# Kernel optimization log

Measured on AMD Instinct MI355X. Metric: run time of the kernel, lower is better.

## Reference

```python
import jax, jax.numpy as jnp
import numpy as np
import math

D = 128  # embedding_dim, hard-coded in source


def setup_inputs() -> dict:
    key = jax.random.key(0)
    k1, k2, k3, k4, k5 = jax.random.split(key, 5)
    B, S = 4, 4096
    x = jax.random.normal(k1, (B, S, D), dtype=jnp.float32)
    token_attention_masks = jax.random.randint(k2, (B, S), 0, 2).astype(jnp.int64)
    # torch.rand -> uniform [0,1)
    w_query = jax.random.uniform(k3, (D, D), dtype=jnp.float32)
    w_key = jax.random.uniform(k4, (D, D), dtype=jnp.float32)
    w_value = jax.random.uniform(k5, (D, D), dtype=jnp.float32)
    return {
        "x": x,
        "token_attention_masks": token_attention_masks,
        "w_query": w_query,
        "w_key": w_key,
        "w_value": w_value,
    }


def reference(x, token_attention_masks, w_query, w_key, w_value):
    # QKV projections (single head, no bias)
    query = jnp.einsum('bsd,de->bse', x, w_query)
    key = jnp.einsum('bsd,de,->bse', x, w_key, jnp.float32(1.0)) if False else jnp.einsum('bsd,de->bse', x, w_key)
    value = jnp.einsum('bsd,de->bse', x, w_value)
    dk = key.shape[2]
    scale = jnp.einsum('bqd,bkd->bqk', query, key) / math.sqrt(dk)  # [B,S,S]
    # NOTE: the original module computes an additive mask (`new_scale`) but
    # applies softmax to the UNMASKED `scale` (a bug in the source); we
    # replicate the actual output math faithfully, so the mask is unused.
    attention_probability = jax.nn.softmax(scale, axis=2)
    attention_output = jnp.einsum('bqk,bkd->bqd', attention_probability, value)
    return attention_output
```

## Files before the change

kernel.cpp:

```cpp
#include <hip/hip_runtime.h>
#include <math.h>

#define BATCH  4
#define SEQ    4096
#define DIM    128
#define NROW   (BATCH*SEQ)
#define NSPLIT 8
#define NW     384

typedef _Float16 f16_t;
typedef _Float16 f16x4  __attribute__((ext_vector_type(4)));
typedef _Float16 f16x8  __attribute__((ext_vector_type(8)));
typedef _Float16 f16x16 __attribute__((ext_vector_type(16)));
typedef float    f32x4  __attribute__((ext_vector_type(4)));
typedef float    f32x16 __attribute__((ext_vector_type(16)));

#define QSCALE ((float)(1.4426950408889634 / 11.313708498984761))

__global__ __launch_bounds__(256) void wsplit_kernel(
    const float* __restrict__ wq, const float* __restrict__ wk,
    const float* __restrict__ wv,
    f16_t* __restrict__ Wth, f16_t* __restrict__ Wtl)
{
    const int idx = blockIdx.x*256 + threadIdx.x;
    const int n = idx >> 7;
    const int k = idx & 127;
    const int mat = n >> 7, col = n & 127;
    const float* w = (mat == 0) ? wq : ((mat == 1) ? wk : wv);
    const float v = w[k*DIM + col];
    const f16_t h = (f16_t)v;
    Wth[idx] = h;
    Wtl[idx] = (f16_t)(v - (float)h);
}

#define LDX 72
#define LDE 136

__global__ __launch_bounds__(256) void proj_kernel(
    const float* __restrict__ x,
    const f16_t* __restrict__ Wth, const f16_t* __restrict__ Wtl,
    f16_t* __restrict__ Qh, f16_t* __restrict__ Kh, f16_t* __restrict__ Vt)
{
    __shared__ __align__(16) f16_t smem[(64 + 64 + 128 + 128) * LDX];
    f16_t* sXh = smem;
    f16_t* sXl = smem + 64*LDX;
    f16_t* sWh = smem + 128*LDX;
    f16_t* sWl = smem + 256*LDX;

    const int tid  = threadIdx.x;
    const int wave = tid >> 6;
    const int lane = tid & 63;
    const int quad = lane >> 4;
    const int ln   = lane & 15;

    const int nt = blockIdx.x % 3;
    const int mb = blockIdx.x / 3;
    const int m0 = mb * 64;
    const int n0 = nt * 128;

    f32x4 acc[8];
    #pragma unroll
    for (int nb = 0; nb < 8; nb++)
        for (int r = 0; r < 4; r++) acc[nb][r] = 0.f;

    #pragma unroll
    for (int ph = 0; ph < 2; ph++) {
        __syncthreads();
        #pragma unroll
        for (int i = 0; i < 4; i++) {
            const int idx = tid + 256*i;
            const int r = idx >> 4, f4 = idx & 15;
            const float4 v = *(const float4*)(x + (size_t)(m0+r)*DIM + ph*64 + f4*4);
            f16_t h0=(f16_t)v.x, h1=(f16_t)v.y, h2=(f16_t)v.z, h3=(f16_t)v.w;
            *(f16x4*)(sXh + r*LDX + f4*4) = (f16x4){h0,h1,h2,h3};
            *(f16x4*)(sXl + r*LDX + f4*4) =
                (f16x4){(f16_t)(v.x-(float)h0),(f16_t)(v.y-(float)h1),
                        (f16_t)(v.z-(float)h2),(f16_t)(v.w-(float)h3)};
        }
        #pragma unroll
        for (int i = 0; i < 4; i++) {
            const int idx = tid + 256*i;
            const int n = idx >> 3, g = idx & 7;
            *(uint4*)(sWh + n*LDX + g*8) =
                *(const uint4*)(Wth + (size_t)(n0+n)*DIM + ph*64 + g*8);
            *(uint4*)(sWl + n*LDX + g*8) =
                *(const uint4*)(Wtl + (size_t)(n0+n)*DIM + ph*64 + g*8);
        }
        __syncthreads();

        f16x8 ah[2], al[2];
        #pragma unroll
        for (int ks = 0; ks < 2; ks++) {
            ah[ks] = *(const f16x8*)(sXh + (wave*16+ln)*LDX + quad*8 + ks*32);
            al[ks] = *(const f16x8*)(sXl + (wave*16+ln)*LDX + quad*8 + ks*32);
        }
        #pragma unroll
        for (int nb = 0; nb < 8; nb++) {
            #pragma unroll
            for (int ks = 0; ks < 2; ks++) {
                const f16x8 bh = *(const f16x8*)(sWh + (nb*16+ln)*LDX + quad*8 + ks*32);
                const f16x8 bl = *(const f16x8*)(sWl + (nb*16+ln)*LDX + quad*8 + ks*32);
                acc[nb] = __builtin_amdgcn_mfma_f32_16x16x32_f16(ah[ks], bh, acc[nb], 0,0,0);
                acc[nb] = __builtin_amdgcn_mfma_f32_16x16x32_f16(al[ks], bh, acc[nb], 0,0,0);
                acc[nb] = __builtin_amdgcn_mfma_f32_16x16x32_f16(ah[ks], bl, acc[nb], 0,0,0);
            }
        }
    }

    __syncthreads();

    if (nt != 2) {
        const float scale = (nt == 0) ? QSCALE : 1.0f;
        f16_t* dsth = (nt == 0) ? Qh : Kh;
        f16_t* sH = smem;
        #pragma unroll
        for (int nb = 0; nb < 8; nb++)
            #pragma unroll
            for (int r = 0; r < 4; r++) {
                const int row  = wave*16 + quad*4 + r;
                const int colp = (nb*16 + ln) ^ (quad << 4);
                sH[row*LDE + colp] = (f16_t)(acc[nb][r] * scale);
            }
        __syncthreads();
        #pragma unroll
        for (int jj = 0; jj < 4; jj++) {
            const int c    = tid + 256*jj;
            const int row  = c >> 4;
            const int col  = (c & 15) * 8;
            const int colp = col ^ (((row >> 2) & 3) << 4);
            *(uint4*)(dsth + (size_t)(m0 + row)*DIM + col) =
                *(const uint4*)(sH + row*LDE + colp);
        }
    } else {
        f16_t* svt = smem;
        const int rowl = wave*16 + quad*4;
        #pragma unroll
        for (int nb = 0; nb < 8; nb++)
            for (int r = 0; r < 4; r++)
                svt[(nb*16+ln)*LDX + rowl + r] = (f16_t)acc[nb][r];
        __syncthreads();
        const int bb = m0 >> 12, sloc = m0 & (SEQ-1);
        const int d = tid >> 1, half = tid & 1;
        #pragma unroll
        for (int q = 0; q < 4; q++) {
            *(uint4*)(Vt + ((size_t)bb*DIM + d)*SEQ + sloc + half*32 + q*8) =
                *(const uint4*)(svt + d*LDX + half*32 + q*8);
        }
    }
}

#define LDK 132
#define LDV 68
#define LDO 132

__global__ __launch_bounds__(256, 3) void flash_kernel(
    const f16_t* __restrict__ Qh, const f16_t* __restrict__ Kh,
    const f16_t* __restrict__ Vt,
    f16_t* __restrict__ Opart, float2* __restrict__ mlbuf)
{
    __shared__ __align__(16) f16_t smem[64*LDK + 128*LDV];
    f16_t* sK = smem;
    f16_t* sV = smem + 64*LDK;

    const int tid  = threadIdx.x;
    const int wave = tid >> 6;
    const int lane = tid & 63;
    const int l31  = lane & 31;
    const int h    = lane >> 5;

    const int grp = blockIdx.x & 31;
    const int b   = grp >> 3;
    const int sp  = grp & 7;
    const int qt  = blockIdx.x >> 5;
    const int q0  = qt*128 + wave*32;

    f16x8 qf[8];
    {
        const f16_t* gq = Qh + ((size_t)b*SEQ + q0 + l31)*DIM + h*8;
        #pragma unroll
        for (int ks = 0; ks < 8; ks++)
            qf[ks] = *(const f16x8*)(gq + ks*16);
    }

    f32x16 oacc[4];
    #pragma unroll
    for (int mb = 0; mb < 4; mb++)
        #pragma unroll
        for (int r = 0; r < 16; r++) oacc[mb][r] = 0.f;
    float mrun = -__builtin_inff(), lrun = 0.f;

    const int kr = tid >> 4;
    const int kc = (tid & 15) * 8;
    const int vd = tid >> 3;
    const int vj = (tid & 7) * 8;

    const f16_t* gK = Kh + (size_t)b*SEQ*DIM;
    const f16_t* gV = Vt + (size_t)b*DIM*SEQ;

    for (int kt = sp*8; kt < sp*8 + 8; kt++) {
        float4 pk[4], pv[4];
        {
            const f16_t* gk = gK + (size_t)kt*64*DIM;
            const f16_t* gv = gV + kt*64;
            #pragma unroll
            for (int p = 0; p < 4; p++)
                pk[p] = *(const float4*)(gk + (kr + 16*p)*DIM + kc);
            #pragma unroll
            for (int p = 0; p < 4; p++)
                pv[p] = *(const float4*)(gv + (size_t)(vd + 32*p)*SEQ + vj);
        }
        __syncthreads();
        #pragma unroll
        for (int p = 0; p < 4; p++) {
            const f16x8 w = __builtin_bit_cast(f16x8, pk[p]);
            *(f16x4*)(sK + (kr+16*p)*LDK + kc    ) = __builtin_shufflevector(w, w, 0,1,2,3);
            *(f16x4*)(sK + (kr+16*p)*LDK + kc + 4) = __builtin_shufflevector(w, w, 4,5,6,7);
        }
        #pragma unroll
        for (int p = 0; p < 4; p++) {
            const f16x8 w = __builtin_bit_cast(f16x8, pv[p]);
            *(f16x4*)(sV + (vd+32*p)*LDV + vj    ) = __builtin_shufflevector(w, w, 0,1,2,3);
            *(f16x4*)(sV + (vd+32*p)*LDV + vj + 4) = __builtin_shufflevector(w, w, 4,5,6,7);
        }
        __syncthreads();

        f32x16 sacc[2];
        #pragma unroll
        for (int sb = 0; sb < 2; sb++)
            #pragma unroll
            for (int r = 0; r < 16; r++) sacc[sb][r] = 0.f;
        #pragma unroll
        for (int ks = 0; ks < 8; ks++) {
            #pragma unroll
            for (int sb = 0; sb < 2; sb++) {
                const f16_t* ka = sK + (sb*32 + l31)*LDK + ks*16 + h*8;
                const f16x4 a0 = *(const f16x4*)(ka);
                const f16x4 a1 = *(const f16x4*)(ka + 4);
                const f16x8 af = __builtin_shufflevector(a0, a1, 0,1,2,3,4,5,6,7);
                sacc[sb] = __builtin_amdgcn_mfma_f32_32x32x16_f16(af, qf[ks], sacc[sb], 0,0,0);
            }
        }

        float mx = sacc[0][0];
        #pragma unroll
        for (int sb = 0; sb < 2; sb++)
            #pragma unroll
            for (int r = 0; r < 16; r++) mx = fmaxf(mx, sacc[sb][r]);
        mx = fmaxf(mx, __shfl_xor(mx, 32, 64));
        const float mnew  = fmaxf(mrun, mx);
        const float alpha = exp2f(mrun - mnew);
        mrun = mnew;

        f16x16 pcv[2];
        float rs = 0.f;
        #pragma unroll
        for (int sb = 0; sb < 2; sb++)
            #pragma unroll
            for (int r = 0; r < 16; r++) {
                const float e = exp2f(sacc[sb][r] - mnew);
                rs += e;
                pcv[sb][r] = (f16_t)e;
            }
        rs += __shfl_xor(rs, 32, 64);
        lrun = lrun*alpha + rs;
        #pragma unroll
        for (int mb = 0; mb < 4; mb++)
            #pragma unroll
            for (int r = 0; r < 16; r++) oacc[mb][r] *= alpha;

        #pragma unroll
        for (int t = 0; t < 4; t++) {
            const f16x16 ps = pcv[t>>1];
            const f16x8 pb = (t & 1)
                ? __builtin_shufflevector(ps, ps, 8,9,10,11,12,13,14,15)
                : __builtin_shufflevector(ps, ps, 0,1,2,3,4,5,6,7);
            #pragma unroll
            for (int mb = 0; mb < 4; mb++) {
                const f16_t* va = sV + (mb*32 + l31)*LDV + t*16 + h*4;
                const f16x4 a0 = *(const f16x4*)(va);
                const f16x4 a1 = *(const f16x4*)(va + 8);
                const f16x8 af = __builtin_shufflevector(a0, a1, 0,1,2,3,4,5,6,7);
                oacc[mb] = __builtin_amdgcn_mfma_f32_32x32x16_f16(af, pb, oacc[mb], 0,0,0);
            }
        }
    }

    __syncthreads();
    const float invl = 1.f / lrun;
    f16_t* sOw = smem + wave*32*LDO;
    #pragma unroll
    for (int mb = 0; mb < 4; mb++)
        #pragma unroll
        for (int rp = 0; rp < 8; rp++) {
            const int r0 = rp*2;
            const int d  = mb*32 + (r0 & 3) + 8*(r0 >> 2) + 4*h;
            union { f16_t f[2]; unsigned u; } pkv;
            pkv.f[0] = (f16_t)(oacc[mb][r0]   * invl);
            pkv.f[1] = (f16_t)(oacc[mb][r0+1] * invl);
            *(unsigned*)(sOw + l31*LDO + d) = pkv.u;
        }
    __asm__ volatile("s_waitcnt lgkmcnt(0)" ::: "memory");

    const size_t gb = ((size_t)sp*NROW + (size_t)b*SEQ + q0)*DIM;
    #pragma unroll
    for (int jj = 0; jj < 8; jj++) {
        const int c  = lane + 64*jj;
        const int q  = c >> 4;
        const int dc = (c & 15)*8;
        union { f16x4 v[2]; uint4 u; } o;
        o.v[0] = *(const f16x4*)(sOw + q*LDO + dc);
        o.v[1] = *(const f16x4*)(sOw + q*LDO + dc + 4);
        *(uint4*)(Opart + gb + (size_t)q*DIM + dc) = o.u;
    }
    if (h == 0)
        mlbuf[sp*NROW + b*SEQ + q0 + l31] = make_float2(mrun, lrun);
}

__global__ __launch_bounds__(256) void combine_kernel(
    const f16_t* __restrict__ Opart, const float2* __restrict__ mlbuf,
    float* __restrict__ out)
{
    const int idx = blockIdx.x*256 + threadIdx.x;
    const int row = idx >> 4;
    const int d0  = (idx & 15) * 8;

    float m[NSPLIT], l[NSPLIT];
    #pragma unroll
    for (int s = 0; s < NSPLIT; s++) {
        const float2 v = mlbuf[s*NROW + row];
        m[s] = v.x; l[s] = v.y;
    }
    float M = m[0];
    #pragma unroll
    for (int s = 1; s < NSPLIT; s++) M = fmaxf(M, m[s]);
    float w[NSPLIT], denom = 0.f;
    #pragma unroll
    for (int s = 0; s < NSPLIT; s++) { w[s] = l[s] * exp2f(m[s] - M); denom += w[s]; }
    const float inv = 1.f / denom;

    float o[8] = {0,0,0,0,0,0,0,0};
    #pragma unroll
    for (int s = 0; s < NSPLIT; s++) {
        const f16x8 v = *(const f16x8*)(Opart + ((size_t)s*NROW + row)*DIM + d0);
        const float ws = w[s] * inv;
        #pragma unroll
        for (int j = 0; j < 8; j++) o[j] += ws * (float)v[j];
    }
    float* ob = out + (size_t)row*DIM + d0;
    *(float4*)(ob)     = make_float4(o[0], o[1], o[2], o[3]);
    *(float4*)(ob + 4) = make_float4(o[4], o[5], o[6], o[7]);
}

extern "C" void kernel_launch(void* const* d_in, const int* in_sizes, int n_in,
                              void* d_out, int out_size, void* d_ws, size_t ws_size,
                              hipStream_t stream) {
    const float* x  = (const float*)d_in[0];
    const float* wq = (const float*)d_in[2];
    const float* wk = (const float*)d_in[3];
    const float* wv = (const float*)d_in[4];

    f16_t* ws = (f16_t*)d_ws;
    f16_t* Qh    = ws;
    f16_t* Kh    = Qh  + (size_t)NROW*DIM;
    f16_t* Vt    = Kh  + (size_t)NROW*DIM;
    f16_t* Wth   = Vt  + (size_t)NROW*DIM;
    f16_t* Wtl   = Wth + (size_t)NW*DIM;
    f16_t* Opart = Wtl + (size_t)NW*DIM;
    float2* mlbuf = (float2*)(Opart + (size_t)NSPLIT*NROW*DIM);

    wsplit_kernel <<<NW*DIM/256,            256, 0, stream>>>(wq, wk, wv, Wth, Wtl);
    proj_kernel   <<<(NROW/64)*3,           256, 0, stream>>>(x, Wth, Wtl, Qh, Kh, Vt);
    flash_kernel  <<<BATCH*(SEQ/128)*NSPLIT,256, 0, stream>>>(Qh, Kh, Vt, Opart, mlbuf);
    combine_kernel<<<NROW*DIM/8/256,        256, 0, stream>>>(Opart, mlbuf, (float*)d_out);
}
```

Before: 132.4 us.

## Prefetch next K/V tile into registers, skip redundant rescale, raise occupancy

```diff
diff --git a/kernel.cpp b/kernel.cpp
--- a/kernel.cpp
+++ b/kernel.cpp
@@ -9,6 +9,7 @@
 #define NW     384
 
 typedef _Float16 f16_t;
+typedef _Float16 f16x2  __attribute__((ext_vector_type(2)));
 typedef _Float16 f16x4  __attribute__((ext_vector_type(4)));
 typedef _Float16 f16x8  __attribute__((ext_vector_type(8)));
 typedef _Float16 f16x16 __attribute__((ext_vector_type(16)));
@@ -149,11 +150,11 @@
     }
 }
 
-#define LDK 132
+#define LDK 136
 #define LDV 68
 #define LDO 132
 
-__global__ __launch_bounds__(256, 3) void flash_kernel(
+__global__ __launch_bounds__(256, 4) void flash_kernel(
     const f16_t* __restrict__ Qh, const f16_t* __restrict__ Kh,
     const f16_t* __restrict__ Vt,
     f16_t* __restrict__ Opart, float2* __restrict__ mlbuf)
@@ -197,31 +198,41 @@
     const f16_t* gK = Kh + (size_t)b*SEQ*DIM;
     const f16_t* gV = Vt + (size_t)b*DIM*SEQ;
 
-    for (int kt = sp*8; kt < sp*8 + 8; kt++) {
-        float4 pk[4], pv[4];
-        {
-            const f16_t* gk = gK + (size_t)kt*64*DIM;
-            const f16_t* gv = gV + kt*64;
-            #pragma unroll
-            for (int p = 0; p < 4; p++)
-                pk[p] = *(const float4*)(gk + (kr + 16*p)*DIM + kc);
-            #pragma unroll
-            for (int p = 0; p < 4; p++)
-                pv[p] = *(const float4*)(gv + (size_t)(vd + 32*p)*SEQ + vj);
-        }
-        __syncthreads();
-        #pragma unroll
-        for (int p = 0; p < 4; p++) {
-            const f16x8 w = __builtin_bit_cast(f16x8, pk[p]);
-            *(f16x4*)(sK + (kr+16*p)*LDK + kc    ) = __builtin_shufflevector(w, w, 0,1,2,3);
-            *(f16x4*)(sK + (kr+16*p)*LDK + kc + 4) = __builtin_shufflevector(w, w, 4,5,6,7);
-        }
+    const int kt0 = sp*8, kend = sp*8 + 8;
+
+    float4 pk[4], pv[4];
+    {
+        const f16_t* gk = gK + (size_t)kt0*64*DIM;
+        const f16_t* gv = gV + kt0*64;
+        #pragma unroll
+        for (int p = 0; p < 4; p++)
+            pk[p] = *(const float4*)(gk + (kr + 16*p)*DIM + kc);
+        #pragma unroll
+        for (int p = 0; p < 4; p++)
+            pv[p] = *(const float4*)(gv + (size_t)(vd + 32*p)*SEQ + vj);
+    }
+
+    for (int kt = kt0; kt < kend; kt++) {
+        __syncthreads();
+        #pragma unroll
+        for (int p = 0; p < 4; p++)
+            *(uint4*)(sK + (kr+16*p)*LDK + kc) = __builtin_bit_cast(uint4, pk[p]);
         #pragma unroll
         for (int p = 0; p < 4; p++) {
             const f16x8 w = __builtin_bit_cast(f16x8, pv[p]);
             *(f16x4*)(sV + (vd+32*p)*LDV + vj    ) = __builtin_shufflevector(w, w, 0,1,2,3);
             *(f16x4*)(sV + (vd+32*p)*LDV + vj + 4) = __builtin_shufflevector(w, w, 4,5,6,7);
         }
+        if (kt + 1 < kend) {
+            const f16_t* gk = gK + (size_t)(kt+1)*64*DIM;
+            const f16_t* gv = gV + (kt+1)*64;
+            #pragma unroll
+            for (int p = 0; p < 4; p++)
+                pk[p] = *(const float4*)(gk + (kr + 16*p)*DIM + kc);
+            #pragma unroll
+            for (int p = 0; p < 4; p++)
+                pv[p] = *(const float4*)(gv + (size_t)(vd + 32*p)*SEQ + vj);
+        }
         __syncthreads();
 
         f32x16 sacc[2];
@@ -233,10 +244,7 @@
         for (int ks = 0; ks < 8; ks++) {
             #pragma unroll
             for (int sb = 0; sb < 2; sb++) {
-                const f16_t* ka = sK + (sb*32 + l31)*LDK + ks*16 + h*8;
-                const f16x4 a0 = *(const f16x4*)(ka);
-                const f16x4 a1 = *(const f16x4*)(ka + 4);
-                const f16x8 af = __builtin_shufflevector(a0, a1, 0,1,2,3,4,5,6,7);
+                const f16x8 af = *(const f16x8*)(sK + (sb*32 + l31)*LDK + ks*16 + h*8);
                 sacc[sb] = __builtin_amdgcn_mfma_f32_32x32x16_f16(af, qf[ks], sacc[sb], 0,0,0);
             }
         }
@@ -247,33 +255,36 @@
             #pragma unroll
             for (int r = 0; r < 16; r++) mx = fmaxf(mx, sacc[sb][r]);
         mx = fmaxf(mx, __shfl_xor(mx, 32, 64));
-        const float mnew  = fmaxf(mrun, mx);
-        const float alpha = exp2f(mrun - mnew);
-        mrun = mnew;
-
-        f16x16 pcv[2];
+        const float mnew = fmaxf(mrun, mx);
+
+        if (__any(mnew > mrun)) {
+            const float alpha = __builtin_amdgcn_exp2f(mrun - mnew);
+            lrun *= alpha;
+            #pragma unroll
+            for (int mb = 0; mb < 4; mb++)
+                #pragma unroll
+                for (int r = 0; r < 16; r++) oacc[mb][r] *= alpha;
+            mrun = mnew;
+        }
+
+        union PBuf { f16x2 p2[8]; f16x8 v8[2]; } pbf[2];
         float rs = 0.f;
         #pragma unroll
         for (int sb = 0; sb < 2; sb++)
             #pragma unroll
-            for (int r = 0; r < 16; r++) {
-                const float e = exp2f(sacc[sb][r] - mnew);
-                rs += e;
-                pcv[sb][r] = (f16_t)e;
+            for (int r2 = 0; r2 < 8; r2++) {
+                const float e0 = __builtin_amdgcn_exp2f(sacc[sb][2*r2]   - mnew);
+                const float e1 = __builtin_amdgcn_exp2f(sacc[sb][2*r2+1] - mnew);
+                rs += e0 + e1;
+                pbf[sb].p2[r2] = __builtin_bit_cast(f16x2,
+                    __builtin_amdgcn_cvt_pkrtz(e0, e1));
             }
         rs += __shfl_xor(rs, 32, 64);
-        lrun = lrun*alpha + rs;
-        #pragma unroll
-        for (int mb = 0; mb < 4; mb++)
-            #pragma unroll
-            for (int r = 0; r < 16; r++) oacc[mb][r] *= alpha;
+        lrun += rs;
 
         #pragma unroll
         for (int t = 0; t < 4; t++) {
-            const f16x16 ps = pcv[t>>1];
-            const f16x8 pb = (t & 1)
-                ? __builtin_shufflevector(ps, ps, 8,9,10,11,12,13,14,15)
-                : __builtin_shufflevector(ps, ps, 0,1,2,3,4,5,6,7);
+            const f16x8 pb = pbf[t>>1].v8[t&1];
             #pragma unroll
             for (int mb = 0; mb < 4; mb++) {
                 const f16_t* va = sV + (mb*32 + l31)*LDV + t*16 + h*4;
@@ -335,7 +346,10 @@
     for (int s = 1; s < NSPLIT; s++) M = fmaxf(M, m[s]);
     float w[NSPLIT], denom = 0.f;
     #pragma unroll
-    for (int s = 0; s < NSPLIT; s++) { w[s] = l[s] * exp2f(m[s] - M); denom += w[s]; }
+    for (int s = 0; s < NSPLIT; s++) {
+        w[s] = l[s] * __builtin_amdgcn_exp2f(m[s] - M);
+        denom += w[s];
+    }
     const float inv = 1.f / denom;
 
     float o[8] = {0,0,0,0,0,0,0,0};
```

After: 211.1 us. 1.59x slower.
